# Kernel tuning notes

Measured on AMD Instinct MI355X. Metric: run time of the kernel, lower is better.

The kernel has to match this reference:

```python
import jax, jax.numpy as jnp
import numpy as np

D_IN = 200   # 4 * d_embeddings
H = 64       # hidden_size

def setup_inputs() -> dict:
    key = jax.random.key(0)
    ks = jax.random.split(key, 7)
    B, T = 4096, 128
    s_ih = 1.0 / np.sqrt(H)
    x = jax.random.normal(ks[0], (B, T, D_IN), dtype=jnp.float32)
    W_ih = jax.random.uniform(ks[1], (H, D_IN), minval=-s_ih, maxval=s_ih, dtype=jnp.float32)
    W_hh = jax.random.uniform(ks[2], (H, H), minval=-s_ih, maxval=s_ih, dtype=jnp.float32)
    b_ih = jax.random.uniform(ks[3], (H,), minval=-s_ih, maxval=s_ih, dtype=jnp.float32)
    b_hh = jax.random.uniform(ks[4], (H,), minval=-s_ih, maxval=s_ih, dtype=jnp.float32)
    W_out = jax.random.uniform(ks[5], (1, H), minval=-s_ih, maxval=s_ih, dtype=jnp.float32)
    b_out = jax.random.uniform(ks[6], (1,), minval=-s_ih, maxval=s_ih, dtype=jnp.float32)
    return {"x": x, "W_ih": W_ih, "W_hh": W_hh, "b_ih": b_ih, "b_hh": b_hh,
            "W_out": W_out, "b_out": b_out}

def reference(x, W_ih, W_hh, b_ih, b_hh, W_out, b_out):
    B = x.shape[0]
    # precompute input projection for all timesteps: [B, T, H]
    xp = jnp.einsum('btd,hd->bth', x, W_ih) + b_ih + b_hh
    def step(h, xt):
        h = jnp.tanh(xt + h @ W_hh.T)
        return h, None
    h0 = jnp.zeros((B, H), dtype=x.dtype)
    h_last, _ = jax.lax.scan(step, h0, jnp.swapaxes(xp, 0, 1))  # scan over time
    return jax.nn.sigmoid(h_last @ W_out.T + b_out)  # [B, 1]
```

## Files before the change

### kernel.cpp

```cpp
#include <hip/hip_runtime.h>
#include <hip/hip_bf16.h>


#define TSEQ 128
#define DIN  200
#define HID  64
#define NB   8
#define TC   4
#define NCH  (TSEQ/TC)
#define RSTRIDE 804

typedef short bf16x8 __attribute__((ext_vector_type(8)));
typedef float f32x4  __attribute__((ext_vector_type(4)));
typedef const __attribute__((address_space(1))) unsigned int GU32;
typedef __attribute__((address_space(3))) unsigned int LU32;

__device__ __forceinline__ unsigned short f2bf(float f) {
  __hip_bfloat16 h = __float2bfloat16(f);
  return __builtin_bit_cast(unsigned short, h);
}
__device__ __forceinline__ bf16x8 cvt8(f32x4 a, f32x4 b) {
  bf16x8 r;
#pragma unroll
  for (int i = 0; i < 4; ++i) { r[i] = (short)f2bf(a[i]); r[4 + i] = (short)f2bf(b[i]); }
  return r;
}
__device__ __forceinline__ float tanh_fast(float x) {
  float e = exp2f(x * 2.885390081777927f);
  float r = __builtin_amdgcn_rcpf(1.f + e);
  return __builtin_fmaf(-2.f, r, 1.f);
}
__device__ __forceinline__ void barrier_lds() {
  asm volatile("s_waitcnt lgkmcnt(0)" ::: "memory");
  __builtin_amdgcn_s_barrier();
  __builtin_amdgcn_sched_barrier(0);
}
__device__ __forceinline__ void wait_vm8() {
  asm volatile("s_waitcnt vmcnt(8)" ::: "memory");
  __builtin_amdgcn_sched_barrier(0);
}
__device__ __forceinline__ void wait_vm0() {
  asm volatile("s_waitcnt vmcnt(0)" ::: "memory");
  __builtin_amdgcn_sched_barrier(0);
}

__global__ __launch_bounds__(256, 2) void rnn_fused(
    const float* __restrict__ x,   const float* __restrict__ Wih,
    const float* __restrict__ Whh, const float* __restrict__ bih,
    const float* __restrict__ bhh, const float* __restrict__ Wout,
    const float* __restrict__ bout, float* __restrict__ out)
{
  __shared__ float          stg[2][NB][RSTRIDE];
  __shared__ float          xp[TC][NB][68];
  __shared__ unsigned short hbuf[2][16][72];

  const int tid  = threadIdx.x;
  const int w    = tid >> 6;
  const int lane = tid & 63;
  const int m    = lane & 15;
  const int g    = lane >> 4;
  const int b0   = blockIdx.x * NB;

  bf16x8 wihf[4][7];
#pragma unroll
  for (int nt = 0; nt < 4; ++nt) {
    const float* wr = Wih + (size_t)(nt * 16 + m) * DIN;
#pragma unroll
    for (int ks = 0; ks < 7; ++ks) {
      const int d = ks * 32 + g * 8;
      if (d + 8 <= DIN)
        wihf[nt][ks] = cvt8(*reinterpret_cast<const f32x4*>(wr + d),
                            *reinterpret_cast<const f32x4*>(wr + d + 4));
      else
        wihf[nt][ks] = (bf16x8)0;
    }
  }
  bf16x8 whhf[2];
#pragma unroll
  for (int hf = 0; hf < 2; ++hf) {
    const float* wr = Whh + (size_t)(w * 16 + m) * HID + hf * 32 + g * 8;
    whhf[hf] = cvt8(*reinterpret_cast<const f32x4*>(wr),
                    *reinterpret_cast<const f32x4*>(wr + 4));
  }
  float biasv[4];
#pragma unroll
  for (int nt = 0; nt < 4; ++nt) biasv[nt] = bih[nt * 16 + m] + bhh[nt * 16 + m];

  wait_vm0();

  auto LOADC = [&](int buf, int c) {
#pragma unroll
    for (int r = 0; r < 2; ++r) {
      const int row = w * 2 + r;
      const float* gb = x + (size_t)(b0 + row) * (TSEQ * DIN) + (size_t)c * (TC * DIN);
      float* lb = &stg[buf][row][0];
#pragma unroll
      for (int i = 0; i < 3; ++i)
        __builtin_amdgcn_global_load_lds((GU32*)(gb + i * 256 + lane * 4),
                                         (LU32*)(lb + i * 256), 16, 0, 0);
      if (lane < 8)
        __builtin_amdgcn_global_load_lds((GU32*)(gb + 768 + lane * 4),
                                         (LU32*)(lb + 768), 16, 0, 0);
    }
  };
  LOADC(0, 0);
  LOADC(1, 1);

  for (int i = tid; i < 2 * 16 * 72 / 2; i += 256)
    reinterpret_cast<unsigned int*>(&hbuf[0][0][0])[i] = 0u;

  for (int c = 0; c < NCH; ++c) {
    const int buf = c & 1;
    if (c + 1 < NCH) wait_vm8(); else wait_vm0();
    __builtin_amdgcn_s_barrier();
    __builtin_amdgcn_sched_barrier(0);

    bf16x8 afr[7];
    {
      const float* sp = &stg[buf][0][0];
#pragma unroll
      for (int ks = 0; ks < 7; ++ks) {
        const int off = m * RSTRIDE + w * 200 + (ks < 6 ? ks * 32 + g * 8 : 192);
        afr[ks] = cvt8(*reinterpret_cast<const f32x4*>(sp + off),
                       *reinterpret_cast<const f32x4*>(sp + off + 4));
      }
      if (g != 0) afr[6] = (bf16x8)0;
    }
    barrier_lds();

    if (c + 2 < NCH) LOADC(buf, c + 2);

    f32x4 acc[4];
#pragma unroll
    for (int nt = 0; nt < 4; ++nt) acc[nt] = (f32x4)(biasv[nt]);
#pragma unroll
    for (int ks = 0; ks < 7; ++ks)
#pragma unroll
      for (int nt = 0; nt < 4; ++nt)
        acc[nt] = __builtin_amdgcn_mfma_f32_16x16x32_bf16(afr[ks], wihf[nt][ks], acc[nt], 0, 0, 0);
    if (g < 2) {
#pragma unroll
      for (int nt = 0; nt < 4; ++nt)
#pragma unroll
        for (int rr = 0; rr < 4; ++rr)
          xp[w][g * 4 + rr][nt * 16 + m] = acc[nt][rr];
    }
    barrier_lds();

#pragma unroll
    for (int tl = 0; tl < TC; ++tl) {
      const int tt = c * TC + tl;
      const int rb = tt & 1, pb = rb ^ 1;
      bf16x8 ha0 = *reinterpret_cast<const bf16x8*>(&hbuf[pb][m][g * 8]);
      bf16x8 ha1 = *reinterpret_cast<const bf16x8*>(&hbuf[pb][m][32 + g * 8]);
      f32x4 racc;
#pragma unroll
      for (int r = 0; r < 4; ++r) racc[r] = xp[tl][g * 4 + r][w * 16 + m];
      racc = __builtin_amdgcn_mfma_f32_16x16x32_bf16(ha0, whhf[0], racc, 0, 0, 0);
      racc = __builtin_amdgcn_mfma_f32_16x16x32_bf16(ha1, whhf[1], racc, 0, 0, 0);
      if (g < 2) {
#pragma unroll
        for (int r = 0; r < 4; ++r) {
          const float hv = tanh_fast(racc[r]);
          hbuf[rb][g * 4 + r][w * 16 + m] = f2bf(hv);
          if (tt == TSEQ - 1) xp[0][g * 4 + r][w * 16 + m] = hv;
        }
      }
      barrier_lds();
    }
  }

  if (tid < 64) {
    const int b  = lane >> 3;
    const int j0 = (lane & 7) * 8;
    float s = 0.f;
#pragma unroll
    for (int j = 0; j < 8; ++j) s += xp[0][b][j0 + j] * Wout[j0 + j];
    s += __shfl_xor(s, 1, 64);
    s += __shfl_xor(s, 2, 64);
    s += __shfl_xor(s, 4, 64);
    if ((lane & 7) == 0) {
      const float z = s + bout[0];
      out[b0 + b] = __builtin_amdgcn_rcpf(1.f + exp2f(-z * 1.4426950408889634f));
    }
  }
}

extern "C" void kernel_launch(void* const* d_in, const int* in_sizes, int n_in,
                              void* d_out, int out_size, void* d_ws, size_t ws_size,
                              hipStream_t stream) {
  const float* x    = (const float*)d_in[0];
  const float* Wih  = (const float*)d_in[1];
  const float* Whh  = (const float*)d_in[2];
  const float* bih  = (const float*)d_in[3];
  const float* bhh  = (const float*)d_in[4];
  const float* Wout = (const float*)d_in[5];
  const float* bout = (const float*)d_in[6];
  float* out = (float*)d_out;

  const int B = in_sizes[0] / (TSEQ * DIN);
  rnn_fused<<<dim3(B / NB), dim3(256), 0, stream>>>(x, Wih, Whh, bih, bhh, Wout, bout, out);
}
```

Measured before the change: 98.18 us.

## Load x directly into registers, drop LDS staging, double timesteps per chunk

Removes the LDS staging buffer and the async global-to-LDS loads. Each lane now loads its input fragment straight from global memory into registers and prefetches the next chunk while the current MFMAs run. The chunk grows from 4 to 8 timesteps so the 16-row MFMA tile is filled with 8 batches times 2 timesteps, which removes padding waste and halves the input-projection barriers. The hidden-state buffer shrinks to 8 rows. The cost is higher register pressure from the prefetch registers and less coalesced per-lane global loads.

```diff
diff --git a/kernel.cpp b/kernel.cpp
--- a/kernel.cpp
+++ b/kernel.cpp
@@ -6,14 +6,11 @@
 #define DIN  200
 #define HID  64
 #define NB   8
-#define TC   4
+#define TC   8
 #define NCH  (TSEQ/TC)
-#define RSTRIDE 804
 
 typedef short bf16x8 __attribute__((ext_vector_type(8)));
 typedef float f32x4  __attribute__((ext_vector_type(4)));
-typedef const __attribute__((address_space(1))) unsigned int GU32;
-typedef __attribute__((address_space(3))) unsigned int LU32;
 
 __device__ __forceinline__ unsigned short f2bf(float f) {
   __hip_bfloat16 h = __float2bfloat16(f);
@@ -35,14 +32,6 @@
   __builtin_amdgcn_s_barrier();
   __builtin_amdgcn_sched_barrier(0);
 }
-__device__ __forceinline__ void wait_vm8() {
-  asm volatile("s_waitcnt vmcnt(8)" ::: "memory");
-  __builtin_amdgcn_sched_barrier(0);
-}
-__device__ __forceinline__ void wait_vm0() {
-  asm volatile("s_waitcnt vmcnt(0)" ::: "memory");
-  __builtin_amdgcn_sched_barrier(0);
-}
 
 __global__ __launch_bounds__(256, 2) void rnn_fused(
     const float* __restrict__ x,   const float* __restrict__ Wih,
@@ -50,9 +39,8 @@
     const float* __restrict__ bhh, const float* __restrict__ Wout,
     const float* __restrict__ bout, float* __restrict__ out)
 {
-  __shared__ float          stg[2][NB][RSTRIDE];
   __shared__ float          xp[TC][NB][68];
-  __shared__ unsigned short hbuf[2][16][72];
+  __shared__ unsigned short hbuf[2][NB][76];
 
   const int tid  = threadIdx.x;
   const int w    = tid >> 6;
@@ -60,6 +48,25 @@
   const int m    = lane & 15;
   const int g    = lane >> 4;
   const int b0   = blockIdx.x * NB;
+
+  const float* xbase = x + ((size_t)(b0 + (m & 7)) * TSEQ + 2 * w + (m >> 3)) * DIN;
+
+  f32x4 pre[7][2];
+  pre[6][0] = (f32x4)0.f; pre[6][1] = (f32x4)0.f;
+  auto LOADC = [&](int c) {
+    const float* p = xbase + (size_t)c * (TC * DIN);
+#pragma unroll
+    for (int ks = 0; ks < 6; ++ks) {
+      const int d = ks * 32 + g * 8;
+      pre[ks][0] = *reinterpret_cast<const f32x4*>(p + d);
+      pre[ks][1] = *reinterpret_cast<const f32x4*>(p + d + 4);
+    }
+    if (g == 0) {
+      pre[6][0] = *reinterpret_cast<const f32x4*>(p + 192);
+      pre[6][1] = *reinterpret_cast<const f32x4*>(p + 196);
+    }
+  };
+  LOADC(0);
 
   bf16x8 wihf[4][7];
 #pragma unroll
@@ -86,76 +93,39 @@
 #pragma unroll
   for (int nt = 0; nt < 4; ++nt) biasv[nt] = bih[nt * 16 + m] + bhh[nt * 16 + m];
 
-  wait_vm0();
-
-  auto LOADC = [&](int buf, int c) {
-#pragma unroll
-    for (int r = 0; r < 2; ++r) {
-      const int row = w * 2 + r;
-      const float* gb = x + (size_t)(b0 + row) * (TSEQ * DIN) + (size_t)c * (TC * DIN);
-      float* lb = &stg[buf][row][0];
-#pragma unroll
-      for (int i = 0; i < 3; ++i)
-        __builtin_amdgcn_global_load_lds((GU32*)(gb + i * 256 + lane * 4),
-                                         (LU32*)(lb + i * 256), 16, 0, 0);
-      if (lane < 8)
-        __builtin_amdgcn_global_load_lds((GU32*)(gb + 768 + lane * 4),
-                                         (LU32*)(lb + 768), 16, 0, 0);
-    }
-  };
-  LOADC(0, 0);
-  LOADC(1, 1);
-
-  for (int i = tid; i < 2 * 16 * 72 / 2; i += 256)
+  for (int i = tid; i < 608; i += 256)
     reinterpret_cast<unsigned int*>(&hbuf[0][0][0])[i] = 0u;
+  barrier_lds();
 
   for (int c = 0; c < NCH; ++c) {
-    const int buf = c & 1;
-    if (c + 1 < NCH) wait_vm8(); else wait_vm0();
-    __builtin_amdgcn_s_barrier();
-    __builtin_amdgcn_sched_barrier(0);
-
-    bf16x8 afr[7];
-    {
-      const float* sp = &stg[buf][0][0];
-#pragma unroll
-      for (int ks = 0; ks < 7; ++ks) {
-        const int off = m * RSTRIDE + w * 200 + (ks < 6 ? ks * 32 + g * 8 : 192);
-        afr[ks] = cvt8(*reinterpret_cast<const f32x4*>(sp + off),
-                       *reinterpret_cast<const f32x4*>(sp + off + 4));
-      }
-      if (g != 0) afr[6] = (bf16x8)0;
-    }
-    barrier_lds();
-
-    if (c + 2 < NCH) LOADC(buf, c + 2);
-
     f32x4 acc[4];
 #pragma unroll
     for (int nt = 0; nt < 4; ++nt) acc[nt] = (f32x4)(biasv[nt]);
 #pragma unroll
-    for (int ks = 0; ks < 7; ++ks)
+    for (int ks = 0; ks < 7; ++ks) {
+      bf16x8 a = cvt8(pre[ks][0], pre[ks][1]);
 #pragma unroll
       for (int nt = 0; nt < 4; ++nt)
-        acc[nt] = __builtin_amdgcn_mfma_f32_16x16x32_bf16(afr[ks], wihf[nt][ks], acc[nt], 0, 0, 0);
-    if (g < 2) {
+        acc[nt] = __builtin_amdgcn_mfma_f32_16x16x32_bf16(a, wihf[nt][ks], acc[nt], 0, 0, 0);
+    }
+    if (c + 1 < NCH) LOADC(c + 1);
+
 #pragma unroll
-      for (int nt = 0; nt < 4; ++nt)
+    for (int nt = 0; nt < 4; ++nt)
 #pragma unroll
-        for (int rr = 0; rr < 4; ++rr)
-          xp[w][g * 4 + rr][nt * 16 + m] = acc[nt][rr];
-    }
+      for (int rr = 0; rr < 4; ++rr)
+        xp[2 * w + (g >> 1)][(g & 1) * 4 + rr][nt * 16 + m] = acc[nt][rr];
     barrier_lds();
 
 #pragma unroll
     for (int tl = 0; tl < TC; ++tl) {
       const int tt = c * TC + tl;
       const int rb = tt & 1, pb = rb ^ 1;
-      bf16x8 ha0 = *reinterpret_cast<const bf16x8*>(&hbuf[pb][m][g * 8]);
-      bf16x8 ha1 = *reinterpret_cast<const bf16x8*>(&hbuf[pb][m][32 + g * 8]);
+      bf16x8 ha0 = *reinterpret_cast<const bf16x8*>(&hbuf[pb][m & 7][g * 8]);
+      bf16x8 ha1 = *reinterpret_cast<const bf16x8*>(&hbuf[pb][m & 7][32 + g * 8]);
       f32x4 racc;
 #pragma unroll
-      for (int r = 0; r < 4; ++r) racc[r] = xp[tl][g * 4 + r][w * 16 + m];
+      for (int r = 0; r < 4; ++r) racc[r] = xp[tl][(g & 1) * 4 + r][w * 16 + m];
       racc = __builtin_amdgcn_mfma_f32_16x16x32_bf16(ha0, whhf[0], racc, 0, 0, 0);
       racc = __builtin_amdgcn_mfma_f32_16x16x32_bf16(ha1, whhf[1], racc, 0, 0, 0);
       if (g < 2) {
```

Measured after the change: 122.9 us. 1.25x slower.
